# Kernel tuning notes

Measured on AMD Instinct MI355X. Metric: run time of the kernel, lower is better.

The kernel has to match this reference:

```python
import jax, jax.numpy as jnp
import numpy as np
import math

B, T, D, H, FFN_DIM, SE_HID = 16, 1024, 512, 8, 2048, 256
EPS = 1e-5  # torch LayerNorm default


def layer_norm(x, g, b):
    mu = jnp.mean(x, axis=-1, keepdims=True)
    var = jnp.mean((x - mu) ** 2, axis=-1, keepdims=True)
    return (x - mu) * jax.lax.rsqrt(var + EPS) * g + b


def setup_inputs() -> dict:
    key = jax.random.key(0)
    ks = jax.random.split(key, 8)
    s = 0.02
    return {
        "x": jax.random.normal(ks[0], (B, T, D), dtype=jnp.float32),
        "wq": jax.random.normal(ks[1], (D, D), dtype=jnp.float32) * s,
        "wk": jax.random.normal(ks[2], (D, D), dtype=jnp.float32) * s,
        "wv": jax.random.normal(ks[3], (D, D), dtype=jnp.float32) * s,
        "ln1_g": jnp.ones((D,), jnp.float32),
        "ln1_b": jnp.zeros((D,), jnp.float32),
        "se_w1": jax.random.normal(ks[4], (T, SE_HID), dtype=jnp.float32) * s,
        "se_w2": jax.random.normal(ks[5], (SE_HID, T), dtype=jnp.float32) * s,
        "ffn_g": jnp.ones((D,), jnp.float32),
        "ffn_b": jnp.zeros((D,), jnp.float32),
        "w1": jax.random.normal(ks[6], (D, FFN_DIM), dtype=jnp.float32) * s,
        "b1": jnp.zeros((FFN_DIM,), jnp.float32),
        "w2": jax.random.normal(ks[7], (FFN_DIM, D), dtype=jnp.float32) * s,
        "b2": jnp.zeros((D,), jnp.float32),
    }


def _forward(x, wq, wk, wv, ln1_g, ln1_b, se_w1, se_w2, ffn_g, ffn_b, w1, b1, w2, b2):
    # --- SE gate over the sequence axis: squeeze over feature dim D ---
    y = jnp.mean(x, axis=-1)                       # (B, T)
    gate = jax.nn.sigmoid(jax.nn.relu(y @ se_w1) @ se_w2)  # (B, T)
    x = x + x * gate[..., None]

    d = D // H
    n = layer_norm(x, ln1_g, ln1_b)
    q = (n @ wq).reshape(B, T, H, d)
    k = (n @ wk).reshape(B, T, H, d)
    v = (n @ wv).reshape(B, T, H, d)
    attn = jnp.einsum('bnhd,bmhd->bnmh', q, k) / math.sqrt(d)
    w = jax.nn.softmax(attn, axis=2)               # softmax over key dim m
    x = x + jnp.einsum('bnmh,bmhd->bnhd', w, v).reshape(B, T, D)

    # --- FFN (pre-norm, exact GELU as nn.GELU default) ---
    n2 = layer_norm(x, ffn_g, ffn_b)
    h = jax.nn.gelu(n2 @ w1 + b1, approximate=False)
    return x + (h @ w2 + b2)


def reference(x, wq, wk, wv, ln1_g, ln1_b, se_w1, se_w2, ffn_g, ffn_b, w1, b1, w2, b2):
    return _forward(x, wq, wk, wv, ln1_g, ln1_b, se_w1, se_w2, ffn_g, ffn_b, w1, b1, w2, b2)
```

## Files before the change

kernel.cpp:

```cpp
#include <hip/hip_runtime.h>

typedef unsigned int uint32;

using bf16x8 = __attribute__((ext_vector_type(8))) short;
using f32x4  = __attribute__((ext_vector_type(4))) float;

#define B_  16
#define T_  1024
#define D_  512
#define H_  8
#define HD_ 64
#define FFN_ 2048
#define SEH_ 256
#define EPS_ 1e-5f

#define AS1 __attribute__((address_space(1)))
#define AS3 __attribute__((address_space(3)))

__device__ __forceinline__ ushort f2bf(float f) {
  uint32 x = __float_as_uint(f);
  return (ushort)((x + 0x7fffu + ((x >> 16) & 1u)) >> 16);
}
__device__ __forceinline__ float bf2f(ushort u) {
  return __uint_as_float(((uint32)u) << 16);
}
__device__ __forceinline__ uint32 cvtpk(float a, float b) {
  uint32 r;
  asm("v_cvt_pk_bf16_f32 %0, %1, %2" : "=v"(r) : "v"(a), "v"(b));
  return r;
}
__device__ __forceinline__ float gelu_fast(float v) {
  float u = v * (0.7978845608f + 0.0356774081f * v * v);
  float e = __expf(2.0f * u);
  float t = 1.0f - 2.0f * __builtin_amdgcn_rcpf(e + 1.0f);
  return 0.5f * v * (1.0f + t);
}

__global__ __launch_bounds__(256) void cast_transpose_all_k(
    const float* __restrict__ wq, const float* __restrict__ wk,
    const float* __restrict__ wv, const float* __restrict__ w1,
    const float* __restrict__ w2, ushort* __restrict__ wqkvT,
    ushort* __restrict__ w1T, ushort* __restrict__ w2T) {
  __shared__ float tile[32][33];
  int bid = blockIdx.x;
  const float* W; ushort* WT; int K, N, bk, bn;
  if (bid < 768) {
    int w = bid >> 8, r = bid & 255;
    W = (w == 0) ? wq : (w == 1) ? wk : wv;
    WT = wqkvT + (size_t)w * 512 * 512;
    K = 512; N = 512; bk = (r >> 4) * 32; bn = (r & 15) * 32;
  } else if (bid < 1792) {
    int r = bid - 768;
    W = w1; WT = w1T; K = 512; N = 2048; bk = (r >> 6) * 32; bn = (r & 63) * 32;
  } else {
    int r = bid - 1792;
    W = w2; WT = w2T; K = 2048; N = 512; bk = (r >> 4) * 32; bn = (r & 15) * 32;
  }
  int lx = threadIdx.x & 31;
  int ly = threadIdx.x >> 5;
  #pragma unroll
  for (int i = ly; i < 32; i += 8)
    tile[i][lx] = W[(size_t)(bk + i) * N + bn + lx];
  __syncthreads();
  #pragma unroll
  for (int i = ly; i < 32; i += 8)
    WT[(size_t)(bn + i) * K + bk + lx] = f2bf(tile[lx][i]);
}

__global__ __launch_bounds__(256) void se_rowmean_k(const float* __restrict__ x,
                                                    float* __restrict__ y) {
  int row  = blockIdx.x * 4 + (threadIdx.x >> 6);
  int lane = threadIdx.x & 63;
  const float4* p = (const float4*)(x + (size_t)row * D_);
  float4 a = p[lane * 2];
  float4 b = p[lane * 2 + 1];
  float s = a.x + a.y + a.z + a.w + b.x + b.y + b.z + b.w;
  #pragma unroll
  for (int m = 1; m < 64; m <<= 1) s += __shfl_xor(s, m);
  if (lane == 0) y[row] = s * (1.0f / D_);
}

__global__ __launch_bounds__(256) void se_mlp1_k(const float* __restrict__ y,
                                                 const float* __restrict__ w1,
                                                 float* __restrict__ z) {
  __shared__ float yb[T_];
  __shared__ float part[8][32];
  int b = blockIdx.x, jt = blockIdx.y;
  int tid = threadIdx.x;
  #pragma unroll
  for (int i = 0; i < 4; i++) yb[tid + i * 256] = y[(size_t)b * T_ + tid + i * 256];
  __syncthreads();
  int tj = tid & 31, tk = tid >> 5;
  int j = jt * 32 + tj;
  const float* wp = w1 + (size_t)(tk * 128) * SEH_ + j;
  const float* yp = yb + tk * 128;
  float a0 = 0.f, a1 = 0.f, a2 = 0.f, a3 = 0.f;
  #pragma unroll
  for (int t = 0; t < 128; t += 4) {
    a0 += yp[t]     * wp[(t)     * SEH_];
    a1 += yp[t + 1] * wp[(t + 1) * SEH_];
    a2 += yp[t + 2] * wp[(t + 2) * SEH_];
    a3 += yp[t + 3] * wp[(t + 3) * SEH_];
  }
  part[tk][tj] = (a0 + a1) + (a2 + a3);
  __syncthreads();
  if (tid < 32) {
    float s = 0.f;
    #pragma unroll
    for (int k = 0; k < 8; k++) s += part[k][tid];
    z[(size_t)b * SEH_ + jt * 32 + tid] = fmaxf(s, 0.f);
  }
}

__global__ __launch_bounds__(256) void se_mlp2_k(const float* __restrict__ z,
                                                 const float* __restrict__ w2,
                                                 float* __restrict__ gate) {
  __shared__ float zb[SEH_];
  __shared__ float part[2][128];
  int b = blockIdx.x, bt = blockIdx.y;
  int tid = threadIdx.x;
  zb[tid & 255] = z[(size_t)b * SEH_ + (tid & 255)];
  __syncthreads();
  int tt = tid & 127, tk = tid >> 7;
  int t = bt * 128 + tt;
  const float* wp = w2 + (size_t)(tk * 128) * T_ + t;
  const float* zp = zb + tk * 128;
  float a0 = 0.f, a1 = 0.f, a2 = 0.f, a3 = 0.f;
  #pragma unroll
  for (int j = 0; j < 128; j += 4) {
    a0 += zp[j]     * wp[(j)     * T_];
    a1 += zp[j + 1] * wp[(j + 1) * T_];
    a2 += zp[j + 2] * wp[(j + 2) * T_];
    a3 += zp[j + 3] * wp[(j + 3) * T_];
  }
  part[tk][tt] = (a0 + a1) + (a2 + a3);
  __syncthreads();
  if (tid < 128) {
    float s = part[0][tid] + part[1][tid];
    gate[(size_t)b * T_ + bt * 128 + tid] = 1.0f / (1.0f + __expf(-s));
  }
}

__global__ __launch_bounds__(256) void gate_ln1_k(
    const float* __restrict__ x, const float* __restrict__ gate,
    const float* __restrict__ g, const float* __restrict__ beta,
    float* __restrict__ x1, ushort* __restrict__ nbuf) {
  int rid  = blockIdx.x * 4 + (threadIdx.x >> 6);
  int lane = threadIdx.x & 63;
  const float4* xr = (const float4*)(x + (size_t)rid * D_);
  float4 a = xr[lane * 2];
  float4 b = xr[lane * 2 + 1];
  float gv = 1.0f + gate[rid];
  a.x *= gv; a.y *= gv; a.z *= gv; a.w *= gv;
  b.x *= gv; b.y *= gv; b.z *= gv; b.w *= gv;
  float4* x1r = (float4*)(x1 + (size_t)rid * D_);
  x1r[lane * 2]     = a;
  x1r[lane * 2 + 1] = b;
  float s  = a.x + a.y + a.z + a.w + b.x + b.y + b.z + b.w;
  float ss = a.x*a.x + a.y*a.y + a.z*a.z + a.w*a.w + b.x*b.x + b.y*b.y + b.z*b.z + b.w*b.w;
  #pragma unroll
  for (int m = 1; m < 64; m <<= 1) { s += __shfl_xor(s, m); ss += __shfl_xor(ss, m); }
  float mu   = s * (1.0f / D_);
  float var  = ss * (1.0f / D_) - mu * mu;
  float rstd = rsqrtf(var + EPS_);
  const float4* gp = (const float4*)g;
  const float4* bp = (const float4*)beta;
  float4 g0 = gp[lane * 2], g1 = gp[lane * 2 + 1];
  float4 b0 = bp[lane * 2], b1 = bp[lane * 2 + 1];
  union { uint4 v; ushort u[8]; } pk;
  pk.u[0] = f2bf((a.x - mu) * rstd * g0.x + b0.x);
  pk.u[1] = f2bf((a.y - mu) * rstd * g0.y + b0.y);
  pk.u[2] = f2bf((a.z - mu) * rstd * g0.z + b0.z);
  pk.u[3] = f2bf((a.w - mu) * rstd * g0.w + b0.w);
  pk.u[4] = f2bf((b.x - mu) * rstd * g1.x + b1.x);
  pk.u[5] = f2bf((b.y - mu) * rstd * g1.y + b1.y);
  pk.u[6] = f2bf((b.z - mu) * rstd * g1.z + b1.z);
  pk.u[7] = f2bf((b.w - mu) * rstd * g1.w + b1.w);
  *(uint4*)(nbuf + (size_t)rid * D_ + lane * 8) = pk.v;
}

__global__ __launch_bounds__(256) void ln2_k(
    const float* __restrict__ x2, const float* __restrict__ g,
    const float* __restrict__ beta, ushort* __restrict__ nbuf) {
  int rid  = blockIdx.x * 4 + (threadIdx.x >> 6);
  int lane = threadIdx.x & 63;
  const float4* xr = (const float4*)(x2 + (size_t)rid * D_);
  float4 a = xr[lane * 2];
  float4 b = xr[lane * 2 + 1];
  float s  = a.x + a.y + a.z + a.w + b.x + b.y + b.z + b.w;
  float ss = a.x*a.x + a.y*a.y + a.z*a.z + a.w*a.w + b.x*b.x + b.y*b.y + b.z*b.z + b.w*b.w;
  #pragma unroll
  for (int m = 1; m < 64; m <<= 1) { s += __shfl_xor(s, m); ss += __shfl_xor(ss, m); }
  float mu   = s * (1.0f / D_);
  float var  = ss * (1.0f / D_) - mu * mu;
  float rstd = rsqrtf(var + EPS_);
  const float4* gp = (const float4*)g;
  const float4* bp = (const float4*)beta;
  float4 g0 = gp[lane * 2], g1 = gp[lane * 2 + 1];
  float4 b0 = bp[lane * 2], b1 = bp[lane * 2 + 1];
  union { uint4 v; ushort u[8]; } pk;
  pk.u[0] = f2bf((a.x - mu) * rstd * g0.x + b0.x);
  pk.u[1] = f2bf((a.y - mu) * rstd * g0.y + b0.y);
  pk.u[2] = f2bf((a.z - mu) * rstd * g0.z + b0.z);
  pk.u[3] = f2bf((a.w - mu) * rstd * g0.w + b0.w);
  pk.u[4] = f2bf((b.x - mu) * rstd * g1.x + b1.x);
  pk.u[5] = f2bf((b.y - mu) * rstd * g1.y + b1.y);
  pk.u[6] = f2bf((b.z - mu) * rstd * g1.z + b1.z);
  pk.u[7] = f2bf((b.w - mu) * rstd * g1.w + b1.w);
  *(uint4*)(nbuf + (size_t)rid * D_ + lane * 8) = pk.v;
}

#define MFMA16 __builtin_amdgcn_mfma_f32_16x16x32_bf16
template <int BN>
__global__ __launch_bounds__(512, 2) void gemm256_k(
    const ushort* __restrict__ A, const ushort* __restrict__ BT,
    int M, int N, int K,
    const float* __restrict__ bias, const float* __restrict__ resid,
    ushort* __restrict__ outB, ushort* __restrict__ outB2,
    ushort* __restrict__ vTout, float* __restrict__ outF, int epi) {
  constexpr int WNS   = BN / 4;
  constexpr int NT    = BN / 64;
  constexpr int BROWS = BN / 8;
  constexpr int BJ    = BN / 64;
  __shared__ ushort smem[2 * 256 * 64 + 2 * BN * 64];
  ushort* As = smem;
  ushort* Bs = smem + 2 * 256 * 64;

  int tid  = threadIdx.x;
  int wave = tid >> 6;
  int lane = tid & 63;
  int quad = lane >> 4;
  int l15  = lane & 15;
  int wm   = wave >> 2;
  int wn   = wave & 3;
  int lr   = lane >> 3;
  int lcs  = (lane & 7) ^ lr;

  int nbk = N / BN;
  int bid = blockIdx.x;
  int xcd = bid & 7;
  int sb  = bid >> 3;
  int n0  = (sb % nbk) * BN;
  int m0  = ((sb / nbk) * 8 + xcd) * 256;

  f32x4 acc[8][NT];
  #pragma unroll
  for (int i = 0; i < 8; i++)
    #pragma unroll
    for (int j = 0; j < NT; j++) acc[i][j] = (f32x4){0.f, 0.f, 0.f, 0.f};

  const ushort* Ag = A  + (size_t)(m0 + wave * 32 + lr) * K + lcs * 8;
  const ushort* Bg = BT + (size_t)(n0 + wave * BROWS + lr) * K + lcs * 8;

  auto STAGE = [&](int t, int buf) {
    int ko = t * 64;
    ushort* da = As + buf * (256 * 64) + wave * (32 * 64);
    #pragma unroll
    for (int j = 0; j < 4; j++)
      __builtin_amdgcn_global_load_lds((const AS1 void*)(Ag + ko + (size_t)(j * 8) * K),
                                       (AS3 void*)(da + j * 512), 16, 0, 0);
    ushort* db = Bs + buf * (BN * 64) + wave * (BROWS * 64);
    #pragma unroll
    for (int j = 0; j < BJ; j++)
      __builtin_amdgcn_global_load_lds((const AS1 void*)(Bg + ko + (size_t)(j * 8) * K),
                                       (AS3 void*)(db + j * 512), 16, 0, 0);
  };

  int ntt = K >> 6;
  STAGE(0, 0);
  __syncthreads();

  const ushort* Arow = As + (wm * 128 + l15) * 64;
  const ushort* Brow = Bs + (wn * WNS + l15) * 64;
  int c0 = ((0 + quad) ^ (l15 & 7)) * 8;
  int c1 = ((4 + quad) ^ (l15 & 7)) * 8;

  for (int t = 0; t < ntt; ++t) {
    int cur = t & 1;
    if (t + 1 < ntt) STAGE(t + 1, cur ^ 1);
    const ushort* Ab = Arow + cur * (256 * 64);
    const ushort* Bb = Brow + cur * (BN * 64);

    bf16x8 b[NT][2], a[4][2];
    #pragma unroll
    for (int h = 0; h < NT; h++) {
      b[h][0] = *(const bf16x8*)(Bb + h * 1024 + c0);
      b[h][1] = *(const bf16x8*)(Bb + h * 1024 + c1);
    }
    #pragma unroll
    for (int m4 = 0; m4 < 4; m4++) {
      a[m4][0] = *(const bf16x8*)(Ab + m4 * 1024 + c0);
      a[m4][1] = *(const bf16x8*)(Ab + m4 * 1024 + c1);
    }
    #pragma unroll
    for (int m4 = 0; m4 < 4; m4++)
      #pragma unroll
      for (int h = 0; h < NT; h++) {
        acc[m4][h] = MFMA16(a[m4][0], b[h][0], acc[m4][h], 0, 0, 0);
        acc[m4][h] = MFMA16(a[m4][1], b[h][1], acc[m4][h], 0, 0, 0);
      }
    #pragma unroll
    for (int m4 = 0; m4 < 4; m4++) {
      a[m4][0] = *(const bf16x8*)(Ab + (4 + m4) * 1024 + c0);
      a[m4][1] = *(const bf16x8*)(Ab + (4 + m4) * 1024 + c1);
    }
    #pragma unroll
    for (int m4 = 0; m4 < 4; m4++)
      #pragma unroll
      for (int h = 0; h < NT; h++) {
        acc[4 + m4][h] = MFMA16(a[m4][0], b[h][0], acc[4 + m4][h], 0, 0, 0);
        acc[4 + m4][h] = MFMA16(a[m4][1], b[h][1], acc[4 + m4][h], 0, 0, 0);
      }

    __syncthreads();
  }

  int colbase = n0 + wn * WNS;
  if (epi == 2) {
    #pragma unroll
    for (int nt = 0; nt < NT; nt++) {
      int n = colbase + nt * 16 + l15;
      float bv = bias[n];
      #pragma unroll
      for (int mt = 0; mt < 8; mt++) {
        int m = m0 + wm * 128 + mt * 16 + quad * 4;
        #pragma unroll
        for (int r = 0; r < 4; r++) {
          size_t idx = (size_t)(m + r) * N + n;
          outF[idx] = acc[mt][nt][r] + bv + resid[idx];
        }
      }
    }
  } else {
    if (epi == 3 && n0 >= 1024) {
      constexpr int TST = 136;
      ushort* tb = smem + wave * (32 * TST);
      #pragma unroll
      for (int nt = 0; nt < NT; nt++) {
        int dloc = nt * 16 + l15;
        #pragma unroll
        for (int mt = 0; mt < 8; mt++) {
          ushort4 pk;
          pk.x = f2bf(acc[mt][nt][0]);
          pk.y = f2bf(acc[mt][nt][1]);
          pk.z = f2bf(acc[mt][nt][2]);
          pk.w = f2bf(acc[mt][nt][3]);
          *(ushort4*)(tb + dloc * TST + mt * 16 + quad * 4) = pk;
        }
      }
      int dbase = (n0 - 1024) + wn * WNS;
      int bb = m0 >> 10;
      int tg = (m0 & 1023) + wm * 128 + l15 * 8;
      #pragma unroll
      for (int j = 0; j < 8; j++) {
        int dloc = j * 4 + quad;
        int d = dbase + dloc;
        int hh = d >> 6, dd = d & 63;
        uint4 vv = *(const uint4*)(tb + dloc * TST + l15 * 8);
        *(uint4*)(vTout + (((size_t)bb * 8 + hh) * 64 + dd) * 1024 + tg) = vv;
      }
    } else {
      constexpr int RS  = WNS + 8;
      constexpr int LPR = WNS / 8;
      constexpr int RPS = 64 / LPR;
      ushort* tb = smem + wave * (32 * RS);
      ushort* gout; int ldN; float scl;
      if (epi == 1) { gout = outB; ldN = N; scl = 1.0f; }
      else {
        gout = (n0 < 512) ? outB : outB2; ldN = 512;
        scl = (n0 < 512) ? 0.18033688011112042f : 1.0f;
      }
      int ncol = (epi == 1) ? colbase : ((n0 & 511) + wn * WNS);
      float bv[NT];
      #pragma unroll
      for (int nt = 0; nt < NT; nt++)
        bv[nt] = (epi == 1) ? bias[colbase + nt * 16 + l15] : 0.0f;
      int rrow = lane / LPR;
      int seg  = lane % LPR;
      int mrow0 = m0 + wm * 128;
      #pragma unroll
      for (int mtg = 0; mtg < 4; mtg++) {
        #pragma unroll
        for (int mh = 0; mh < 2; mh++) {
          int mt = mtg * 2 + mh;
          #pragma unroll
          for (int nt = 0; nt < NT; nt++) {
            #pragma unroll
            for (int r = 0; r < 4; r++) {
              float v = (epi == 1) ? gelu_fast(acc[mt][nt][r] + bv[nt])
                                   : acc[mt][nt][r] * scl;
              tb[(mh * 16 + quad * 4 + r) * RS + nt * 16 + l15] = f2bf(v);
            }
          }
        }
        #pragma unroll
        for (int it = 0; it < 32 / RPS; it++) {
          int rl = it * RPS + rrow;
          uint4 v = *(const uint4*)(tb + rl * RS + seg * 8);
          *(uint4*)(gout + (size_t)(mrow0 + mtg * 32 + rl) * ldN + ncol + seg * 8) = v;
        }
      }
    }
  }
}

__global__ __launch_bounds__(512, 2) void attn_k(
    const ushort* __restrict__ q, const ushort* __restrict__ k,
    const ushort* __restrict__ vT, const float* __restrict__ x1,
    float* __restrict__ out) {
  __shared__ ushort Ks[2 * 64 * 64];
  __shared__ ushort Vs[2 * 64 * 64];
  __shared__ ushort Ps[256 * 64];
  int bid = blockIdx.x;
  int xcd = bid & 7;
  int j   = bid >> 3;
  int qt  = j & 3;
  int pair = xcd * 16 + (j >> 2);
  int b = pair >> 3;
  int h = pair & 7;
  int t0 = qt * 256;
  int tid  = threadIdx.x;
  int wave = tid >> 6;
  int lane = tid & 63;
  int quad = lane >> 4;
  int l15  = lane & 15;

  int row8 = lane >> 3;
  int csw  = ((lane & 7) ^ row8) * 8;
  const ushort* kst = k + ((size_t)(b * T_ + wave * 8 + row8)) * D_ + h * HD_ + csw;
  const ushort* vst = vT + ((size_t)((b * 8 + h) * 64 + wave * 8 + row8)) * 1024 + csw;
  ushort* KsW = Ks + wave * 512;
  ushort* VsW = Vs + wave * 512;

  auto STAGE = [&](int kt, int buf) {
    __builtin_amdgcn_global_load_lds((const AS1 void*)(kst + (size_t)kt * 64 * D_),
                                     (AS3 void*)(KsW + buf * 4096), 16, 0, 0);
    __builtin_amdgcn_global_load_lds((const AS1 void*)(vst + kt * 64),
                                     (AS3 void*)(VsW + buf * 4096), 16, 0, 0);
  };

  STAGE(0, 0);

  const ushort* qp0 = q + ((size_t)(b * T_ + t0 + wave * 16 + l15)) * D_ + h * HD_;
  const ushort* qp1 = qp0 + (size_t)128 * D_;
  bf16x8 aq0 = *(const bf16x8*)(qp0 + quad * 8);
  bf16x8 aq1 = *(const bf16x8*)(qp0 + 32 + quad * 8);
  bf16x8 aq2 = *(const bf16x8*)(qp1 + quad * 8);
  bf16x8 aq3 = *(const bf16x8*)(qp1 + 32 + quad * 8);

  int rsw0 = ((quad)     ^ (l15 & 7)) << 3;
  int rsw1 = ((quad + 4) ^ (l15 & 7)) << 3;

  float l_part[2][4] = {{0.f, 0.f, 0.f, 0.f}, {0.f, 0.f, 0.f, 0.f}};
  f32x4 o0[4], o1[4];
  #pragma unroll
  for (int dt = 0; dt < 4; dt++) {
    o0[dt] = (f32x4){0.f, 0.f, 0.f, 0.f};
    o1[dt] = (f32x4){0.f, 0.f, 0.f, 0.f};
  }

  asm volatile("s_waitcnt vmcnt(0)" ::: "memory");
  __syncthreads();

  for (int kt = 0; kt < 16; kt++) {
    int buf = kt & 1;
    if (kt + 1 < 16) STAGE(kt + 1, buf ^ 1);
    const ushort* Kb = Ks + buf * 4096;
    const ushort* Vb = Vs + buf * 4096;

    #pragma unroll
    for (int nt = 0; nt < 4; nt++) {
      const ushort* krow = Kb + (nt * 16 + l15) * 64;
      bf16x8 bk0 = *(const bf16x8*)(krow + rsw0);
      bf16x8 bk1 = *(const bf16x8*)(krow + rsw1);
      f32x4 z = (f32x4){0.f, 0.f, 0.f, 0.f};
      f32x4 s0 = MFMA16(aq0, bk0, z, 0, 0, 0);
      s0 = MFMA16(aq1, bk1, s0, 0, 0, 0);
      f32x4 s1 = MFMA16(aq2, bk0, z, 0, 0, 0);
      s1 = MFMA16(aq3, bk1, s1, 0, 0, 0);

      float p0[4], p1[4];
      #pragma unroll
      for (int r = 0; r < 4; r++) {
        p0[r] = __builtin_amdgcn_exp2f(s0[r]);
        p1[r] = __builtin_amdgcn_exp2f(s1[r]);
        l_part[0][r] += p0[r];
        l_part[1][r] += p1[r];
      }
      int cps = nt * 2 + (l15 >> 3);
      int cbase = l15 & 7;
      #pragma unroll
      for (int hs = 0; hs < 2; hs++) {
        uint32 u01 = cvtpk(hs ? p1[0] : p0[0], hs ? p1[1] : p0[1]);
        uint32 u23 = cvtpk(hs ? p1[2] : p0[2], hs ? p1[3] : p0[3]);
        int rb = hs * 128 + wave * 16 + quad * 4;
        #pragma unroll
        for (int r = 0; r < 4; r++) {
          int off = (rb + r) * 64 + ((cps ^ ((quad * 4 + r) & 7)) << 3) + cbase;
          uint32 uu = (r < 2) ? u01 : u23;
          Ps[off] = (ushort)((r & 1) ? (uu >> 16) : uu);
        }
      }
    }

    const ushort* prow = Ps + (wave * 16 + l15) * 64;
    bf16x8 ap0 = *(const bf16x8*)(prow + rsw0);
    bf16x8 ap1 = *(const bf16x8*)(prow + rsw1);
    bf16x8 ap2 = *(const bf16x8*)(prow + 8192 + rsw0);
    bf16x8 ap3 = *(const bf16x8*)(prow + 8192 + rsw1);
    #pragma unroll
    for (int dt = 0; dt < 4; dt++) {
      const ushort* vrow = Vb + (dt * 16 + l15) * 64;
      bf16x8 bv0 = *(const bf16x8*)(vrow + rsw0);
      bf16x8 bv1 = *(const bf16x8*)(vrow + rsw1);
      o0[dt] = MFMA16(ap0, bv0, o0[dt], 0, 0, 0);
      o0[dt] = MFMA16(ap1, bv1, o0[dt], 0, 0, 0);
      o1[dt] = MFMA16(ap2, bv0, o1[dt], 0, 0, 0);
      o1[dt] = MFMA16(ap3, bv1, o1[dt], 0, 0, 0);
    }

    __syncthreads();
  }

  #pragma unroll
  for (int s = 0; s < 2; s++) {
    f32x4* oo = s ? o1 : o0;
    #pragma unroll
    for (int r = 0; r < 4; r++) {
      float l = l_part[s][r];
      l += __shfl_xor(l, 1);
      l += __shfl_xor(l, 2);
      l += __shfl_xor(l, 4);
      l += __shfl_xor(l, 8);
      float inv = 1.0f / l;
      int qrow = t0 + s * 128 + wave * 16 + quad * 4 + r;
      size_t base = ((size_t)(b * T_ + qrow)) * D_ + h * HD_;
      #pragma unroll
      for (int dt = 0; dt < 4; dt++) {
        size_t idx = base + dt * 16 + l15;
        out[idx] = x1[idx] + oo[dt][r] * inv;
      }
    }
  }
}

extern "C" void kernel_launch(void* const* d_in, const int* in_sizes, int n_in,
                              void* d_out, int out_size, void* d_ws, size_t ws_size,
                              hipStream_t stream) {
  (void)in_sizes; (void)n_in; (void)out_size; (void)ws_size;
  const float* x     = (const float*)d_in[0];
  const float* wq    = (const float*)d_in[1];
  const float* wk    = (const float*)d_in[2];
  const float* wv    = (const float*)d_in[3];
  const float* ln1_g = (const float*)d_in[4];
  const float* ln1_b = (const float*)d_in[5];
  const float* se_w1 = (const float*)d_in[6];
  const float* se_w2 = (const float*)d_in[7];
  const float* ffn_g = (const float*)d_in[8];
  const float* ffn_b = (const float*)d_in[9];
  const float* w1    = (const float*)d_in[10];
  const float* b1    = (const float*)d_in[11];
  const float* w2    = (const float*)d_in[12];
  const float* b2    = (const float*)d_in[13];
  float* out = (float*)d_out;
  char* ws = (char*)d_ws;

  constexpr size_t X1_OFF   = 0;
  constexpr size_t N_OFF    = 33554432;
  constexpr size_t Q_OFF    = 50331648;
  constexpr size_t K_OFF    = 67108864;
  constexpr size_t V_OFF    = 83886080;
  constexpr size_t H_OFF    = 50331648;
  constexpr size_t WQKV_OFF = 117440512;
  constexpr size_t W1T_OFF  = 119013376;
  constexpr size_t W2T_OFF  = 121110528;
  constexpr size_t Y_OFF    = 123207680;
  constexpr size_t Z_OFF    = 123273216;
  constexpr size_t GATE_OFF = 123289600;

  float*  x1    = (float*)(ws + X1_OFF);
  ushort* nbuf  = (ushort*)(ws + N_OFF);
  ushort* qb    = (ushort*)(ws + Q_OFF);
  ushort* kb    = (ushort*)(ws + K_OFF);
  ushort* vT    = (ushort*)(ws + V_OFF);
  ushort* hb    = (ushort*)(ws + H_OFF);
  ushort* wqkvT = (ushort*)(ws + WQKV_OFF);
  ushort* w1T   = (ushort*)(ws + W1T_OFF);
  ushort* w2T   = (ushort*)(ws + W2T_OFF);
  float*  yv    = (float*)(ws + Y_OFF);
  float*  zv    = (float*)(ws + Z_OFF);
  float*  gate  = (float*)(ws + GATE_OFF);

  const int M = B_ * T_;

  cast_transpose_all_k<<<2816, 256, 0, stream>>>(wq, wk, wv, w1, w2, wqkvT, w1T, w2T);

  se_rowmean_k<<<M / 4, 256, 0, stream>>>(x, yv);
  se_mlp1_k<<<dim3(B_, 8), 256, 0, stream>>>(yv, se_w1, zv);
  se_mlp2_k<<<dim3(B_, 8), 256, 0, stream>>>(zv, se_w2, gate);

  gate_ln1_k<<<M / 4, 256, 0, stream>>>(x, gate, ln1_g, ln1_b, x1, nbuf);

  gemm256_k<128><<<(M / 256) * (1536 / 128), 512, 0, stream>>>(
      nbuf, wqkvT, M, 1536, D_, nullptr, nullptr, qb, kb, vT, nullptr, 3);

  attn_k<<<B_ * H_ * (T_ / 256), 512, 0, stream>>>(qb, kb, vT, x1, out);

  ln2_k<<<M / 4, 256, 0, stream>>>(out, ffn_g, ffn_b, nbuf);

  gemm256_k<256><<<(M / 256) * (FFN_ / 256), 512, 0, stream>>>(
      nbuf, w1T, M, FFN_, D_, b1, nullptr, hb, nullptr, nullptr, nullptr, 1);
  gemm256_k<128><<<(M / 256) * (D_ / 128), 512, 0, stream>>>(
      hb, w2T, M, D_, FFN_, b2, out, nullptr, nullptr, nullptr, out, 2);
}
```

Before: 309.0 us.

## Replace templated GEMM with triple-buffered 256x128 tile kernel using fine-grained waitcnt

All three GEMMs now use one 256x128 block tile with a 4x2 wave layout, where each wave computes a 64x64 subtile. Loads are triple-buffered: the kernel prefetches two K-steps ahead and uses explicit vmcnt waits with raw barriers instead of a full __syncthreads every iteration. The aim is to hide global-to-LDS latency better and to shrink per-wave accumulator state. In exchange, the FFN1 GEMM gives up its wider 256-column tile, and the larger LDS footprint drops the launch-bounds occupancy hint to one block per CU.

```diff
diff --git a/kernel.cpp b/kernel.cpp
--- a/kernel.cpp
+++ b/kernel.cpp
@@ -211,119 +211,114 @@
 }
 
 #define MFMA16 __builtin_amdgcn_mfma_f32_16x16x32_bf16
-template <int BN>
-__global__ __launch_bounds__(512, 2) void gemm256_k(
+__global__ __launch_bounds__(512, 1) void gemm128_k(
     const ushort* __restrict__ A, const ushort* __restrict__ BT,
     int M, int N, int K,
     const float* __restrict__ bias, const float* __restrict__ resid,
     ushort* __restrict__ outB, ushort* __restrict__ outB2,
     ushort* __restrict__ vTout, float* __restrict__ outF, int epi) {
-  constexpr int WNS   = BN / 4;
-  constexpr int NT    = BN / 64;
-  constexpr int BROWS = BN / 8;
-  constexpr int BJ    = BN / 64;
-  __shared__ ushort smem[2 * 256 * 64 + 2 * BN * 64];
+  constexpr int AT = 256 * 64;
+  constexpr int BTL = 128 * 64;
+  __shared__ ushort smem[3 * AT + 3 * BTL];
   ushort* As = smem;
-  ushort* Bs = smem + 2 * 256 * 64;
+  ushort* Bs = smem + 3 * AT;
 
   int tid  = threadIdx.x;
   int wave = tid >> 6;
   int lane = tid & 63;
   int quad = lane >> 4;
   int l15  = lane & 15;
-  int wm   = wave >> 2;
-  int wn   = wave & 3;
+  int wm   = wave >> 1;
+  int wn   = wave & 1;
   int lr   = lane >> 3;
   int lcs  = (lane & 7) ^ lr;
 
-  int nbk = N / BN;
+  int nbk = N >> 7;
   int bid = blockIdx.x;
   int xcd = bid & 7;
   int sb  = bid >> 3;
-  int n0  = (sb % nbk) * BN;
+  int n0  = (sb % nbk) * 128;
   int m0  = ((sb / nbk) * 8 + xcd) * 256;
 
-  f32x4 acc[8][NT];
-  #pragma unroll
-  for (int i = 0; i < 8; i++)
-    #pragma unroll
-    for (int j = 0; j < NT; j++) acc[i][j] = (f32x4){0.f, 0.f, 0.f, 0.f};
+  f32x4 acc[4][4];
+  #pragma unroll
+  for (int i = 0; i < 4; i++)
+    #pragma unroll
+    for (int j = 0; j < 4; j++) acc[i][j] = (f32x4){0.f, 0.f, 0.f, 0.f};
 
   const ushort* Ag = A  + (size_t)(m0 + wave * 32 + lr) * K + lcs * 8;
-  const ushort* Bg = BT + (size_t)(n0 + wave * BROWS + lr) * K + lcs * 8;
+  const ushort* Bg = BT + (size_t)(n0 + wave * 16 + lr) * K + lcs * 8;
 
   auto STAGE = [&](int t, int buf) {
     int ko = t * 64;
-    ushort* da = As + buf * (256 * 64) + wave * (32 * 64);
+    ushort* da = As + buf * AT + wave * (32 * 64);
     #pragma unroll
     for (int j = 0; j < 4; j++)
       __builtin_amdgcn_global_load_lds((const AS1 void*)(Ag + ko + (size_t)(j * 8) * K),
                                        (AS3 void*)(da + j * 512), 16, 0, 0);
-    ushort* db = Bs + buf * (BN * 64) + wave * (BROWS * 64);
-    #pragma unroll
-    for (int j = 0; j < BJ; j++)
+    ushort* db = Bs + buf * BTL + wave * (16 * 64);
+    #pragma unroll
+    for (int j = 0; j < 2; j++)
       __builtin_amdgcn_global_load_lds((const AS1 void*)(Bg + ko + (size_t)(j * 8) * K),
                                        (AS3 void*)(db + j * 512), 16, 0, 0);
   };
 
   int ntt = K >> 6;
   STAGE(0, 0);
-  __syncthreads();
-
-  const ushort* Arow = As + (wm * 128 + l15) * 64;
-  const ushort* Brow = Bs + (wn * WNS + l15) * 64;
+  STAGE(1, 1);
+  asm volatile("s_waitcnt vmcnt(6)" ::: "memory");
+  __builtin_amdgcn_s_barrier();
+
   int c0 = ((0 + quad) ^ (l15 & 7)) * 8;
   int c1 = ((4 + quad) ^ (l15 & 7)) * 8;
+  int cur = 0;
 
   for (int t = 0; t < ntt; ++t) {
-    int cur = t & 1;
-    if (t + 1 < ntt) STAGE(t + 1, cur ^ 1);
-    const ushort* Ab = Arow + cur * (256 * 64);
-    const ushort* Bb = Brow + cur * (BN * 64);
-
-    bf16x8 b[NT][2], a[4][2];
-    #pragma unroll
-    for (int h = 0; h < NT; h++) {
-      b[h][0] = *(const bf16x8*)(Bb + h * 1024 + c0);
-      b[h][1] = *(const bf16x8*)(Bb + h * 1024 + c1);
-    }
-    #pragma unroll
-    for (int m4 = 0; m4 < 4; m4++) {
-      a[m4][0] = *(const bf16x8*)(Ab + m4 * 1024 + c0);
-      a[m4][1] = *(const bf16x8*)(Ab + m4 * 1024 + c1);
-    }
-    #pragma unroll
-    for (int m4 = 0; m4 < 4; m4++)
-      #pragma unroll
-      for (int h = 0; h < NT; h++) {
-        acc[m4][h] = MFMA16(a[m4][0], b[h][0], acc[m4][h], 0, 0, 0);
-        acc[m4][h] = MFMA16(a[m4][1], b[h][1], acc[m4][h], 0, 0, 0);
-      }
-    #pragma unroll
-    for (int m4 = 0; m4 < 4; m4++) {
-      a[m4][0] = *(const bf16x8*)(Ab + (4 + m4) * 1024 + c0);
-      a[m4][1] = *(const bf16x8*)(Ab + (4 + m4) * 1024 + c1);
-    }
-    #pragma unroll
-    for (int m4 = 0; m4 < 4; m4++)
-      #pragma unroll
-      for (int h = 0; h < NT; h++) {
-        acc[4 + m4][h] = MFMA16(a[m4][0], b[h][0], acc[4 + m4][h], 0, 0, 0);
-        acc[4 + m4][h] = MFMA16(a[m4][1], b[h][1], acc[4 + m4][h], 0, 0, 0);
-      }
-
-    __syncthreads();
-  }
-
-  int colbase = n0 + wn * WNS;
+    int nx2 = cur + 2; if (nx2 >= 3) nx2 -= 3;
+    if (t + 2 < ntt) STAGE(t + 2, nx2);
+    const ushort* Ab = As + cur * AT + (wm * 64 + l15) * 64;
+    const ushort* Bb = Bs + cur * BTL + (wn * 64 + l15) * 64;
+
+    bf16x8 a[4][2], b[4][2];
+    #pragma unroll
+    for (int nt = 0; nt < 4; nt++) {
+      b[nt][0] = *(const bf16x8*)(Bb + nt * 1024 + c0);
+      b[nt][1] = *(const bf16x8*)(Bb + nt * 1024 + c1);
+    }
+    #pragma unroll
+    for (int mt = 0; mt < 4; mt++) {
+      a[mt][0] = *(const bf16x8*)(Ab + mt * 1024 + c0);
+      a[mt][1] = *(const bf16x8*)(Ab + mt * 1024 + c1);
+    }
+    #pragma unroll
+    for (int mt = 0; mt < 4; mt++)
+      #pragma unroll
+      for (int nt = 0; nt < 4; nt++)
+        acc[mt][nt] = MFMA16(a[mt][0], b[nt][0], acc[mt][nt], 0, 0, 0);
+    #pragma unroll
+    for (int mt = 0; mt < 4; mt++)
+      #pragma unroll
+      for (int nt = 0; nt < 4; nt++)
+        acc[mt][nt] = MFMA16(a[mt][1], b[nt][1], acc[mt][nt], 0, 0, 0);
+
+    if (t + 1 < ntt) {
+      if (t + 2 < ntt) asm volatile("s_waitcnt vmcnt(6)" ::: "memory");
+      else             asm volatile("s_waitcnt vmcnt(0)" ::: "memory");
+      __builtin_amdgcn_s_barrier();
+    }
+    cur = cur + 1 == 3 ? 0 : cur + 1;
+  }
+
+  int colbase = n0 + wn * 64;
+  int mrow0   = m0 + wm * 64;
   if (epi == 2) {
     #pragma unroll
-    for (int nt = 0; nt < NT; nt++) {
+    for (int nt = 0; nt < 4; nt++) {
       int n = colbase + nt * 16 + l15;
       float bv = bias[n];
       #pragma unroll
-      for (int mt = 0; mt < 8; mt++) {
-        int m = m0 + wm * 128 + mt * 16 + quad * 4;
+      for (int mt = 0; mt < 4; mt++) {
+        int m = mrow0 + mt * 16 + quad * 4;
         #pragma unroll
         for (int r = 0; r < 4; r++) {
           size_t idx = (size_t)(m + r) * N + n;
@@ -332,14 +327,15 @@
       }
     }
   } else {
+    __syncthreads();
     if (epi == 3 && n0 >= 1024) {
-      constexpr int TST = 136;
-      ushort* tb = smem + wave * (32 * TST);
-      #pragma unroll
-      for (int nt = 0; nt < NT; nt++) {
+      constexpr int TST = 72;
+      ushort* tb = smem + wave * (64 * TST);
+      #pragma unroll
+      for (int nt = 0; nt < 4; nt++) {
         int dloc = nt * 16 + l15;
         #pragma unroll
-        for (int mt = 0; mt < 8; mt++) {
+        for (int mt = 0; mt < 4; mt++) {
           ushort4 pk;
           pk.x = f2bf(acc[mt][nt][0]);
           pk.y = f2bf(acc[mt][nt][1]);
@@ -348,21 +344,19 @@
           *(ushort4*)(tb + dloc * TST + mt * 16 + quad * 4) = pk;
         }
       }
-      int dbase = (n0 - 1024) + wn * WNS;
+      int dbase = (n0 - 1024) + wn * 64;
       int bb = m0 >> 10;
-      int tg = (m0 & 1023) + wm * 128 + l15 * 8;
-      #pragma unroll
-      for (int j = 0; j < 8; j++) {
-        int dloc = j * 4 + quad;
+      int tg = (m0 & 1023) + wm * 64 + (lane & 7) * 8;
+      #pragma unroll
+      for (int it = 0; it < 8; it++) {
+        int dloc = it * 8 + (lane >> 3);
         int d = dbase + dloc;
         int hh = d >> 6, dd = d & 63;
-        uint4 vv = *(const uint4*)(tb + dloc * TST + l15 * 8);
+        uint4 vv = *(const uint4*)(tb + dloc * TST + (lane & 7) * 8);
         *(uint4*)(vTout + (((size_t)bb * 8 + hh) * 64 + dd) * 1024 + tg) = vv;
       }
     } else {
-      constexpr int RS  = WNS + 8;
-      constexpr int LPR = WNS / 8;
-      constexpr int RPS = 64 / LPR;
+      constexpr int RS = 72;
       ushort* tb = smem + wave * (32 * RS);
       ushort* gout; int ldN; float scl;
       if (epi == 1) { gout = outB; ldN = N; scl = 1.0f; }
@@ -370,34 +364,33 @@
         gout = (n0 < 512) ? outB : outB2; ldN = 512;
         scl = (n0 < 512) ? 0.18033688011112042f : 1.0f;
       }
-      int ncol = (epi == 1) ? colbase : ((n0 & 511) + wn * WNS);
-      float bv[NT];
-      #pragma unroll
-      for (int nt = 0; nt < NT; nt++)
+      int ncol = (epi == 1) ? colbase : ((n0 & 511) + wn * 64);
+      float bv[4];
+      #pragma unroll
+      for (int nt = 0; nt < 4; nt++)
         bv[nt] = (epi == 1) ? bias[colbase + nt * 16 + l15] : 0.0f;
-      int rrow = lane / LPR;
-      int seg  = lane % LPR;
-      int mrow0 = m0 + wm * 128;
-      #pragma unroll
-      for (int mtg = 0; mtg < 4; mtg++) {
+      int rrow = lane >> 3;
+      int seg  = lane & 7;
+      #pragma unroll
+      for (int rh = 0; rh < 2; rh++) {
         #pragma unroll
-        for (int mh = 0; mh < 2; mh++) {
-          int mt = mtg * 2 + mh;
+        for (int m2 = 0; m2 < 2; m2++) {
+          int mt = rh * 2 + m2;
           #pragma unroll
-          for (int nt = 0; nt < NT; nt++) {
+          for (int nt = 0; nt < 4; nt++) {
             #pragma unroll
             for (int r = 0; r < 4; r++) {
               float v = (epi == 1) ? gelu_fast(acc[mt][nt][r] + bv[nt])
                                    : acc[mt][nt][r] * scl;
-              tb[(mh * 16 + quad * 4 + r) * RS + nt * 16 + l15] = f2bf(v);
+              tb[(m2 * 16 + quad * 4 + r) * RS + nt * 16 + l15] = f2bf(v);
             }
           }
         }
         #pragma unroll
-        for (int it = 0; it < 32 / RPS; it++) {
-          int rl = it * RPS + rrow;
+        for (int it = 0; it < 4; it++) {
+          int rl = it * 8 + rrow;
           uint4 v = *(const uint4*)(tb + rl * RS + seg * 8);
-          *(uint4*)(gout + (size_t)(mrow0 + mtg * 32 + rl) * ldN + ncol + seg * 8) = v;
+          *(uint4*)(gout + (size_t)(mrow0 + rh * 32 + rl) * ldN + ncol + seg * 8) = v;
         }
       }
     }
@@ -601,15 +594,15 @@
 
   gate_ln1_k<<<M / 4, 256, 0, stream>>>(x, gate, ln1_g, ln1_b, x1, nbuf);
 
-  gemm256_k<128><<<(M / 256) * (1536 / 128), 512, 0, stream>>>(
+  gemm128_k<<<(M / 256) * (1536 / 128), 512, 0, stream>>>(
       nbuf, wqkvT, M, 1536, D_, nullptr, nullptr, qb, kb, vT, nullptr, 3);
 
   attn_k<<<B_ * H_ * (T_ / 256), 512, 0, stream>>>(qb, kb, vT, x1, out);
 
   ln2_k<<<M / 4, 256, 0, stream>>>(out, ffn_g, ffn_b, nbuf);
 
-  gemm256_k<256><<<(M / 256) * (FFN_ / 256), 512, 0, stream>>>(
+  gemm128_k<<<(M / 256) * (FFN_ / 128), 512, 0, stream>>>(
       nbuf, w1T, M, FFN_, D_, b1, nullptr, hb, nullptr, nullptr, nullptr, 1);
-  gemm256_k<128><<<(M / 256) * (D_ / 128), 512, 0, stream>>>(
+  gemm128_k<<<(M / 256) * (D_ / 128), 512, 0, stream>>>(
       hb, w2T, M, D_, FFN_, b2, out, nullptr, nullptr, nullptr, out, 2);
 }
```

Result: slower. 320.8 us (+3.8%).

## Add 256x128 K=32 GEMM kernel for QKV and FFN1 projections

Applied to the files above, without the earlier changes.

Introduces a new GEMM kernel with a 256x128 tile and a 32-wide K step, using per-wave direct global-to-LDS loads with an XOR-swizzled layout and double buffering. It replaces the larger templated GEMM for the QKV and FFN-up projections, which have K=512. The templated kernel keeps only the residual-add epilogue for FFN-down and drops to one block per CU in its launch bounds. The smaller tile with fewer accumulators is meant to allow two blocks per CU and more blocks in the grid, at the cost of less data reuse per tile and a barrier every 32 K.

```diff
diff --git a/kernel.cpp b/kernel.cpp
--- a/kernel.cpp
+++ b/kernel.cpp
@@ -211,13 +211,167 @@
 }
 
 #define MFMA16 __builtin_amdgcn_mfma_f32_16x16x32_bf16
+
+__global__ __launch_bounds__(512, 2) void gemm32_k(
+    const ushort* __restrict__ A, const ushort* __restrict__ BT,
+    int M, int N, int K, const float* __restrict__ bias,
+    ushort* __restrict__ outB, ushort* __restrict__ outB2,
+    ushort* __restrict__ vTout, int epi) {
+  constexpr int ATile = 8192;
+  constexpr int BTile = 4096;
+  __shared__ ushort smem[2 * ATile + 2 * BTile];
+  ushort* As = smem;
+  ushort* Bs = smem + 2 * ATile;
+
+  int tid  = threadIdx.x;
+  int wave = tid >> 6;
+  int lane = tid & 63;
+  int quad = lane >> 4;
+  int l15  = lane & 15;
+  int wm   = wave >> 1;
+  int wn   = wave & 1;
+
+  int p0  = (lane & 7) ^ (lane >> 3);
+  int rlo = 2 * (lane >> 3) + (p0 >> 2);
+  int kc8 = (p0 & 3) * 8;
+
+  int nbk = N >> 7;
+  int bid = blockIdx.x;
+  int xcd = bid & 7;
+  int sb  = bid >> 3;
+  int n0  = (sb % nbk) * 128;
+  int m0  = ((sb / nbk) * 8 + xcd) * 256;
+
+  f32x4 acc[4][4];
+  #pragma unroll
+  for (int i = 0; i < 4; i++)
+    #pragma unroll
+    for (int j = 0; j < 4; j++) acc[i][j] = (f32x4){0.f, 0.f, 0.f, 0.f};
+
+  const ushort* Ag = A  + (size_t)(m0 + rlo) * K + kc8;
+  const ushort* Bg = BT + (size_t)(n0 + rlo) * K + kc8;
+  ushort* AsW = As + wave * 1024;
+  ushort* BsW = Bs + wave * 512;
+
+  auto STAGE = [&](int kt, int buf) {
+    const ushort* a0 = Ag + (size_t)(wave * 32) * K + kt * 32;
+    __builtin_amdgcn_global_load_lds((const AS1 void*)a0,
+                                     (AS3 void*)(AsW + buf * ATile), 16, 0, 0);
+    __builtin_amdgcn_global_load_lds((const AS1 void*)(a0 + (size_t)16 * K),
+                                     (AS3 void*)(AsW + buf * ATile + 512), 16, 0, 0);
+    __builtin_amdgcn_global_load_lds((const AS1 void*)(Bg + (size_t)(wave * 16) * K + kt * 32),
+                                     (AS3 void*)(BsW + buf * BTile), 16, 0, 0);
+  };
+
+  int ntt = K >> 5;
+  STAGE(0, 0);
+  __syncthreads();
+
+  int lbase = (l15 >> 1) * 64 + ((((l15 & 1) << 2) + quad) ^ ((l15 >> 1) & 7)) * 8;
+  const ushort* Arow = As + wm * 2048 + lbase;
+  const ushort* Brow = Bs + wn * 2048 + lbase;
+
+  for (int t = 0; t < ntt; ++t) {
+    int cur = t & 1;
+    if (t + 1 < ntt) STAGE(t + 1, cur ^ 1);
+    const ushort* Ab = Arow + cur * ATile;
+    const ushort* Bb = Brow + cur * BTile;
+
+    bf16x8 a[4], b[4];
+    #pragma unroll
+    for (int g = 0; g < 4; g++) b[g] = *(const bf16x8*)(Bb + g * 512);
+    #pragma unroll
+    for (int f = 0; f < 4; f++) a[f] = *(const bf16x8*)(Ab + f * 512);
+    #pragma unroll
+    for (int f = 0; f < 4; f++)
+      #pragma unroll
+      for (int g = 0; g < 4; g++)
+        acc[f][g] = MFMA16(a[f], b[g], acc[f][g], 0, 0, 0);
+
+    __syncthreads();
+  }
+
+  int colbase = n0 + wn * 64;
+  int mrow0   = m0 + wm * 64;
+  __syncthreads();
+  if (epi == 3 && n0 >= 1024) {
+    constexpr int TST = 72;
+    ushort* tb = smem + wave * (32 * TST);
+    int dbase = (n0 - 1024) + wn * 64;
+    int bb = m0 >> 10;
+    int tg = (m0 & 1023) + wm * 64 + (lane & 7) * 8;
+    #pragma unroll
+    for (int hf = 0; hf < 2; hf++) {
+      #pragma unroll
+      for (int n2 = 0; n2 < 2; n2++) {
+        int nt = hf * 2 + n2;
+        int dloc = n2 * 16 + l15;
+        #pragma unroll
+        for (int mt = 0; mt < 4; mt++) {
+          ushort4 pk;
+          pk.x = f2bf(acc[mt][nt][0]);
+          pk.y = f2bf(acc[mt][nt][1]);
+          pk.z = f2bf(acc[mt][nt][2]);
+          pk.w = f2bf(acc[mt][nt][3]);
+          *(ushort4*)(tb + dloc * TST + mt * 16 + quad * 4) = pk;
+        }
+      }
+      #pragma unroll
+      for (int it = 0; it < 4; it++) {
+        int dl = it * 8 + (lane >> 3);
+        int d = dbase + hf * 32 + dl;
+        int hh = d >> 6, dd = d & 63;
+        uint4 vv = *(const uint4*)(tb + dl * TST + (lane & 7) * 8);
+        *(uint4*)(vTout + (((size_t)bb * 8 + hh) * 64 + dd) * 1024 + tg) = vv;
+      }
+    }
+  } else {
+    constexpr int RS = 72;
+    ushort* tb = smem + wave * (32 * RS);
+    ushort* gout; int ldN; float scl;
+    if (epi == 1) { gout = outB; ldN = N; scl = 1.0f; }
+    else {
+      gout = (n0 < 512) ? outB : outB2; ldN = 512;
+      scl = (n0 < 512) ? 0.18033688011112042f : 1.0f;
+    }
+    int ncol = (epi == 1) ? colbase : ((n0 & 511) + wn * 64);
+    float bv[4];
+    #pragma unroll
+    for (int nt = 0; nt < 4; nt++)
+      bv[nt] = (epi == 1) ? bias[colbase + nt * 16 + l15] : 0.0f;
+    int rrow = lane >> 3;
+    int seg  = lane & 7;
+    #pragma unroll
+    for (int rh = 0; rh < 2; rh++) {
+      #pragma unroll
+      for (int m2 = 0; m2 < 2; m2++) {
+        int mt = rh * 2 + m2;
+        #pragma unroll
+        for (int nt = 0; nt < 4; nt++) {
+          #pragma unroll
+          for (int r = 0; r < 4; r++) {
+            float v = (epi == 1) ? gelu_fast(acc[mt][nt][r] + bv[nt])
+                                 : acc[mt][nt][r] * scl;
+            tb[(m2 * 16 + quad * 4 + r) * RS + nt * 16 + l15] = f2bf(v);
+          }
+        }
+      }
+      #pragma unroll
+      for (int it = 0; it < 4; it++) {
+        int rl = it * 8 + rrow;
+        uint4 v = *(const uint4*)(tb + rl * RS + seg * 8);
+        *(uint4*)(gout + (size_t)(mrow0 + rh * 32 + rl) * ldN + ncol + seg * 8) = v;
+      }
+    }
+  }
+}
+
 template <int BN>
-__global__ __launch_bounds__(512, 2) void gemm256_k(
+__global__ __launch_bounds__(512, 1) void gemm256_k(
     const ushort* __restrict__ A, const ushort* __restrict__ BT,
     int M, int N, int K,
     const float* __restrict__ bias, const float* __restrict__ resid,
-    ushort* __restrict__ outB, ushort* __restrict__ outB2,
-    ushort* __restrict__ vTout, float* __restrict__ outF, int epi) {
+    float* __restrict__ outF) {
   constexpr int WNS   = BN / 4;
   constexpr int NT    = BN / 64;
   constexpr int BROWS = BN / 8;
@@ -316,89 +470,17 @@
   }
 
   int colbase = n0 + wn * WNS;
-  if (epi == 2) {
-    #pragma unroll
-    for (int nt = 0; nt < NT; nt++) {
-      int n = colbase + nt * 16 + l15;
-      float bv = bias[n];
-      #pragma unroll
-      for (int mt = 0; mt < 8; mt++) {
-        int m = m0 + wm * 128 + mt * 16 + quad * 4;
-        #pragma unroll
-        for (int r = 0; r < 4; r++) {
-          size_t idx = (size_t)(m + r) * N + n;
-          outF[idx] = acc[mt][nt][r] + bv + resid[idx];
-        }
-      }
-    }
-  } else {
-    if (epi == 3 && n0 >= 1024) {
-      constexpr int TST = 136;
-      ushort* tb = smem + wave * (32 * TST);
-      #pragma unroll
-      for (int nt = 0; nt < NT; nt++) {
-        int dloc = nt * 16 + l15;
-        #pragma unroll
-        for (int mt = 0; mt < 8; mt++) {
-          ushort4 pk;
-          pk.x = f2bf(acc[mt][nt][0]);
-          pk.y = f2bf(acc[mt][nt][1]);
-          pk.z = f2bf(acc[mt][nt][2]);
-          pk.w = f2bf(acc[mt][nt][3]);
-          *(ushort4*)(tb + dloc * TST + mt * 16 + quad * 4) = pk;
-        }
-      }
-      int dbase = (n0 - 1024) + wn * WNS;
-      int bb = m0 >> 10;
-      int tg = (m0 & 1023) + wm * 128 + l15 * 8;
-      #pragma unroll
-      for (int j = 0; j < 8; j++) {
-        int dloc = j * 4 + quad;
-        int d = dbase + dloc;
-        int hh = d >> 6, dd = d & 63;
-        uint4 vv = *(const uint4*)(tb + dloc * TST + l15 * 8);
-        *(uint4*)(vTout + (((size_t)bb * 8 + hh) * 64 + dd) * 1024 + tg) = vv;
-      }
-    } else {
-      constexpr int RS  = WNS + 8;
-      constexpr int LPR = WNS / 8;
-      constexpr int RPS = 64 / LPR;
-      ushort* tb = smem + wave * (32 * RS);
-      ushort* gout; int ldN; float scl;
-      if (epi == 1) { gout = outB; ldN = N; scl = 1.0f; }
-      else {
-        gout = (n0 < 512) ? outB : outB2; ldN = 512;
-        scl = (n0 < 512) ? 0.18033688011112042f : 1.0f;
-      }
-      int ncol = (epi == 1) ? colbase : ((n0 & 511) + wn * WNS);
-      float bv[NT];
-      #pragma unroll
-      for (int nt = 0; nt < NT; nt++)
-        bv[nt] = (epi == 1) ? bias[colbase + nt * 16 + l15] : 0.0f;
-      int rrow = lane / LPR;
-      int seg  = lane % LPR;
-      int mrow0 = m0 + wm * 128;
-      #pragma unroll
-      for (int mtg = 0; mtg < 4; mtg++) {
-        #pragma unroll
-        for (int mh = 0; mh < 2; mh++) {
-          int mt = mtg * 2 + mh;
-          #pragma unroll
-          for (int nt = 0; nt < NT; nt++) {
-            #pragma unroll
-            for (int r = 0; r < 4; r++) {
-              float v = (epi == 1) ? gelu_fast(acc[mt][nt][r] + bv[nt])
-                                   : acc[mt][nt][r] * scl;
-              tb[(mh * 16 + quad * 4 + r) * RS + nt * 16 + l15] = f2bf(v);
-            }
-          }
-        }
-        #pragma unroll
-        for (int it = 0; it < 32 / RPS; it++) {
-          int rl = it * RPS + rrow;
-          uint4 v = *(const uint4*)(tb + rl * RS + seg * 8);
-          *(uint4*)(gout + (size_t)(mrow0 + mtg * 32 + rl) * ldN + ncol + seg * 8) = v;
-        }
+  #pragma unroll
+  for (int nt = 0; nt < NT; nt++) {
+    int n = colbase + nt * 16 + l15;
+    float bv = bias[n];
+    #pragma unroll
+    for (int mt = 0; mt < 8; mt++) {
+      int m = m0 + wm * 128 + mt * 16 + quad * 4;
+      #pragma unroll
+      for (int r = 0; r < 4; r++) {
+        size_t idx = (size_t)(m + r) * N + n;
+        outF[idx] = acc[mt][nt][r] + bv + resid[idx];
       }
     }
   }
@@ -601,15 +683,15 @@
 
   gate_ln1_k<<<M / 4, 256, 0, stream>>>(x, gate, ln1_g, ln1_b, x1, nbuf);
 
-  gemm256_k<128><<<(M / 256) * (1536 / 128), 512, 0, stream>>>(
-      nbuf, wqkvT, M, 1536, D_, nullptr, nullptr, qb, kb, vT, nullptr, 3);
+  gemm32_k<<<(M / 256) * (1536 / 128), 512, 0, stream>>>(
+      nbuf, wqkvT, M, 1536, D_, nullptr, qb, kb, vT, 3);
 
   attn_k<<<B_ * H_ * (T_ / 256), 512, 0, stream>>>(qb, kb, vT, x1, out);
 
   ln2_k<<<M / 4, 256, 0, stream>>>(out, ffn_g, ffn_b, nbuf);
 
-  gemm256_k<256><<<(M / 256) * (FFN_ / 256), 512, 0, stream>>>(
-      nbuf, w1T, M, FFN_, D_, b1, nullptr, hb, nullptr, nullptr, nullptr, 1);
+  gemm32_k<<<(M / 256) * (FFN_ / 128), 512, 0, stream>>>(
+      nbuf, w1T, M, FFN_, D_, b1, hb, nullptr, nullptr, 1);
   gemm256_k<128><<<(M / 256) * (D_ / 128), 512, 0, stream>>>(
-      hb, w2T, M, D_, FFN_, b2, out, nullptr, nullptr, nullptr, out, 2);
-}
+      hb, w2T, M, D_, FFN_, b2, out, out);
+}
```

After: 317.1 us. 2.6% more time.
